# Kernel optimization log

Hardware: AMD Instinct MI355X
Metric: run time of the kernel (lower is better)

Reference implementation:

```python
import jax, jax.numpy as jnp
import numpy as np

LEAKY_ALPHA = 0.2
EPS_NORM = 1e-07


def _leaky_relu(x):
    return jnp.where(x >= 0, x, LEAKY_ALPHA * x)


def setup_inputs() -> dict:
    key = jax.random.key(0)
    ks = jax.random.split(key, 10)
    B, N, F = 16, 1024, 256
    H, Q, K, V = 4, 128, 128, 128
    return {
        "e": jax.random.normal(ks[0], (B, N, N), dtype=jnp.float32),
        "x_atm": jax.random.normal(ks[1], (B, N, F), dtype=jnp.float32),
        "mask": jnp.ones((B, N), dtype=jnp.float32),
        "eps": jax.random.normal(ks[2], (1,), dtype=jnp.float32) * 0.02,
        "Wq": jax.random.normal(ks[3], (H, F, Q), dtype=jnp.float32) * 0.05,
        "Wk": jax.random.normal(ks[4], (H, F, K), dtype=jnp.float32) * 0.05,
        "Wv": jax.random.normal(ks[5], (H, F, V), dtype=jnp.float32) * 0.05,
        "aq": jax.random.normal(ks[6], (H, Q), dtype=jnp.float32) * 0.05,
        "bq": jnp.zeros((H,), dtype=jnp.float32),
        "ak": jax.random.normal(ks[7], (H, K), dtype=jnp.float32) * 0.05,
        "bk": jnp.zeros((H,), dtype=jnp.float32),
    }


def reference(e, x_atm, mask, eps, Wq, Wk, Wv, aq, bq, ak, bk):
    B, N, _ = e.shape
    # add learned eps to the diagonal of e (set_diag(diag + eps))
    e_mod = e + eps[0] * jnp.eye(N, dtype=e.dtype)  # [B,N,N]

    # per-head query/key scalars: Dense -> LeakyReLU -> Dense(1)
    q = jnp.einsum("bhnq,hq->bhn", _leaky_relu(jnp.einsum("bnf,hfq->bhnq", x_atm, Wq)), aq) + bq[None, :, None]  # [B,H,N]
    k = jnp.einsum("bhnk,hk->bhn", _leaky_relu(jnp.einsum("bnf,hfk->bhnk", x_atm, Wk)), ak) + bk[None, :, None]  # [B,H,N]

    # attn[b,h,i,j] = tanh((q_i + k_j) * e_mod[b,i,j])
    scores = jnp.tanh((q[..., :, None] + k[..., None, :]) * e_mod[:, None, :, :])  # [B,H,N,N]

    # L2-normalize each row (tf.linalg.normalize norm + 1e-7)
    norm = jnp.sqrt(jnp.sum(scores * scores, axis=-1, keepdims=True)) + EPS_NORM
    attn = scores / norm

    # values and aggregation
    v = jnp.einsum("bnf,hfv->bhnv", x_atm, Wv)  # [B,H,N,V] (dropout rate 0 -> identity)
    out = jnp.einsum("bhij,bhjv->bhiv", attn, v)  # [B,H,N,V]

    # pooling == 'mask': sum over nodes weighted by mask -> [B,H,V]
    pooled = jnp.einsum("bhnv,bn->bhv", out, mask)

    # concat heads along feature axis -> [B, H*V]
    return pooled.reshape(B, -1)
```

## Files before the change

kernel.cpp:

```cpp
#include <hip/hip_runtime.h>

#define B_ 16
#define N_ 1024
#define F_ 256
#define H_ 4
#define QDIM 128

#define TANH_PRESCALE 2.8853900817779268f

typedef __attribute__((ext_vector_type(8))) short bf16x8;
typedef __attribute__((ext_vector_type(4))) float f32x4;

__device__ __forceinline__ float leaky(float x) {
    return x >= 0.f ? x : 0.2f * x;
}

__device__ __forceinline__ unsigned short bfbits(float f) {
    unsigned u = __float_as_uint(f);
    return (unsigned short)((u + 0x7fffu + ((u >> 16) & 1u)) >> 16);
}

__global__ __launch_bounds__(256) void convert_all(
    const float4* __restrict__ x4, ushort4* __restrict__ xh4,
    const float* __restrict__ Wq, const float* __restrict__ Wk,
    ushort* __restrict__ Wqt, ushort* __restrict__ Wkt)
{
    const int bx = blockIdx.x;
    if (bx < 2048) {
        const int t = bx * 256 + threadIdx.x;
        const float4 a = x4[2 * t], b = x4[2 * t + 1];
        ushort4 o0, o1;
        o0.x = bfbits(a.x); o0.y = bfbits(a.y); o0.z = bfbits(a.z); o0.w = bfbits(a.w);
        o1.x = bfbits(b.x); o1.y = bfbits(b.y); o1.z = bfbits(b.z); o1.w = bfbits(b.w);
        xh4[2 * t] = o0; xh4[2 * t + 1] = o1;
    } else {
        const int t2 = (bx - 2048) * 256 + threadIdx.x;
        const int z = t2 >> 17, t = t2 & 131071;
        const int f = t & 255, q = (t >> 8) & 127, h = t >> 15;
        const float* W = z ? Wk : Wq;
        ushort* O = z ? Wkt : Wqt;
        O[t] = bfbits(W[(h * 256 + f) * 128 + q]);
    }
}

__global__ __launch_bounds__(256) void qk_mfma(
    const ushort* __restrict__ xh,
    const ushort* __restrict__ Wqt, const ushort* __restrict__ Wkt,
    const float* __restrict__ aq, const float* __restrict__ bq,
    const float* __restrict__ ak, const float* __restrict__ bk,
    float* __restrict__ qbuf, float* __restrict__ kbuf)
{
    const int tid = threadIdx.x;
    const int mt  = blockIdx.x;
    const int h   = blockIdx.y;
    const bool isQ = (blockIdx.z == 0);
    const ushort* Wt = isQ ? Wqt : Wkt;
    const float*  av = isQ ? aq : ak;
    const float*  bv = isQ ? bq : bk;
    float* out = isQ ? qbuf : kbuf;

    __shared__ char  xs[64 * 512];
    __shared__ float sp[4][64];

    {
        const int r = tid >> 2;
        const uint4* src = reinterpret_cast<const uint4*>(xh + (size_t)(mt * 64 + r) * 256);
        #pragma unroll
        for (int i = 0; i < 8; ++i) {
            const int c = (tid & 3) + 4 * i;
            const uint4 v = src[c];
            *reinterpret_cast<uint4*>(xs + r * 512 + ((c ^ (r & 7)) << 4)) = v;
        }
    }
    __syncthreads();

    const int l  = tid & 63, w = tid >> 6;
    const int g  = l >> 4, li = l & 15;

    bf16x8 Bf[8][2];
    #pragma unroll
    for (int nf = 0; nf < 2; ++nf) {
        const int c = w * 32 + nf * 16 + li;
        const ushort* bp = Wt + ((size_t)(h * 128 + c)) * 256 + 8 * g;
        #pragma unroll
        for (int s = 0; s < 8; ++s)
            Bf[s][nf] = *reinterpret_cast<const bf16x8*>(bp + s * 32);
    }

    f32x4 acc[4][2];
    #pragma unroll
    for (int m = 0; m < 4; ++m)
        #pragma unroll
        for (int nf = 0; nf < 2; ++nf)
            acc[m][nf] = (f32x4){0.f, 0.f, 0.f, 0.f};

    #pragma unroll
    for (int s = 0; s < 8; ++s) {
        #pragma unroll
        for (int m = 0; m < 4; ++m) {
            const int r = m * 16 + li;
            const int chunk = (4 * s + g) ^ (r & 7);
            const bf16x8 af = *reinterpret_cast<const bf16x8*>(xs + r * 512 + chunk * 16);
            acc[m][0] = __builtin_amdgcn_mfma_f32_16x16x32_bf16(af, Bf[s][0], acc[m][0], 0, 0, 0);
            acc[m][1] = __builtin_amdgcn_mfma_f32_16x16x32_bf16(af, Bf[s][1], acc[m][1], 0, 0, 0);
        }
    }

    float part[4][4];
    #pragma unroll
    for (int m = 0; m < 4; ++m)
        #pragma unroll
        for (int j = 0; j < 4; ++j) part[m][j] = 0.f;

    #pragma unroll
    for (int nf = 0; nf < 2; ++nf) {
        const float a_ = av[h * QDIM + w * 32 + nf * 16 + li];
        #pragma unroll
        for (int m = 0; m < 4; ++m)
            #pragma unroll
            for (int j = 0; j < 4; ++j)
                part[m][j] = fmaf(a_, leaky(acc[m][nf][j]), part[m][j]);
    }
    #pragma unroll
    for (int mask = 1; mask < 16; mask <<= 1)
        #pragma unroll
        for (int m = 0; m < 4; ++m)
            #pragma unroll
            for (int j = 0; j < 4; ++j)
                part[m][j] += __shfl_xor(part[m][j], mask, 64);

    if (li == 0) {
        #pragma unroll
        for (int m = 0; m < 4; ++m)
            #pragma unroll
            for (int j = 0; j < 4; ++j)
                sp[w][m * 16 + g * 4 + j] = part[m][j];
    }
    __syncthreads();

    if (tid < 64) {
        const float val = (sp[0][tid] + sp[1][tid] + sp[2][tid] + sp[3][tid] + bv[h]) * TANH_PRESCALE;
        const int R = mt * 64 + tid;
        out[((R >> 10) * H_ + h) * N_ + (R & 1023)] = val;
    }
}

__global__ __launch_bounds__(512) void attn_kernel(
    const float* __restrict__ e,
    const float* __restrict__ qbuf, const float* __restrict__ kbuf,
    const float* __restrict__ mask, const float* __restrict__ epsp,
    float* __restrict__ pbuf)
{
    const int tid  = threadIdx.x;
    const int wav  = tid >> 6;
    const int h    = wav & 3;
    const int half = wav >> 2;
    const int lane = tid & 63;
    const int b    = blockIdx.y;
    const int ic   = blockIdx.x;
    const int i0   = ic * 16 + half * 8;
    const float epsv = epsp[0];
    const int udiag = ic >> 4;

    __shared__ f32x4 red4[4][4][64];

    const f32x4* kr4 = reinterpret_cast<const f32x4*>(kbuf + (b * H_ + h) * N_);
    f32x4 kk4[4];
    #pragma unroll
    for (int u = 0; u < 4; ++u) kk4[u] = kr4[u * 64 + lane];

    f32x4 wacc4[4];
    #pragma unroll
    for (int u = 0; u < 4; ++u) wacc4[u] = (f32x4){0.f, 0.f, 0.f, 0.f};

    const float* qrow  = qbuf + (b * H_ + h) * N_;
    const float* mrow  = mask + b * N_;
    const f32x4* ebase = reinterpret_cast<const f32x4*>(e + ((size_t)b << 20)) + lane;

    #pragma unroll 2
    for (int ii = 0; ii < 8; ++ii) {
        const int i = i0 + ii;
        const float qi = qrow[i];
        const f32x4* er4 = ebase + ((size_t)i << 8);
        const bool isdl = (lane == ((i >> 2) & 63));
        const float dadd = isdl ? epsv : 0.f;
        float p[4][4];
        float ssl = 0.f;
        #pragma unroll
        for (int u = 0; u < 4; ++u) {
            const f32x4 ev = er4[u * 64];
            const f32x4 kv = kk4[u];
            #pragma unroll
            for (int c = 0; c < 4; ++c) {
                const float qk = qi + kv[c];
                float arg = qk * ev[c];
                if (u == udiag && c == (ii & 3)) arg = fmaf(qk, dadd, arg);
                const float e2 = __builtin_amdgcn_exp2f(arg);
                const float pv = 1.f - 2.f * __builtin_amdgcn_rcpf(e2 + 1.f);
                p[u][c] = pv;
                ssl = fmaf(pv, pv, ssl);
            }
        }
        #pragma unroll
        for (int m = 1; m < 64; m <<= 1) ssl += __shfl_xor(ssl, m, 64);
        const float scale = mrow[i] * __builtin_amdgcn_rcpf(sqrtf(ssl) + 1e-7f);
        #pragma unroll
        for (int u = 0; u < 4; ++u)
            #pragma unroll
            for (int c = 0; c < 4; ++c)
                wacc4[u][c] = fmaf(scale, p[u][c], wacc4[u][c]);
    }

    if (half == 1) {
        #pragma unroll
        for (int u = 0; u < 4; ++u) red4[h][u][lane] = wacc4[u];
    }
    __syncthreads();
    if (half == 0) {
        f32x4* pr4 = reinterpret_cast<f32x4*>(pbuf + ((size_t)((ic * 16 + b) * H_ + h) << 10));
        #pragma unroll
        for (int u = 0; u < 4; ++u) {
            const f32x4 o = wacc4[u] + red4[h][u][lane];
            pr4[u * 64 + lane] = o;
        }
    }
}

__global__ __launch_bounds__(256) void ypart_kernel(
    const float* __restrict__ x, const float* __restrict__ pbuf,
    float* __restrict__ ypart)
{
    const int tid = threadIdx.x;
    const int bx  = blockIdx.x;
    const int b   = bx >> 4;
    const int jc  = bx & 15;
    const int j0  = jc * 64;

    __shared__ float ws_[H_][64];
    {
        const int hh = tid >> 6, j = tid & 63;
        const float* pp = pbuf + ((size_t)(b * H_ + hh) << 10) + j0 + j;
        float s0 = 0.f, s1 = 0.f, s2 = 0.f, s3 = 0.f;
        #pragma unroll 4
        for (int ic = 0; ic < 64; ic += 4) {
            s0 += pp[(size_t)(ic + 0) * 65536];
            s1 += pp[(size_t)(ic + 1) * 65536];
            s2 += pp[(size_t)(ic + 2) * 65536];
            s3 += pp[(size_t)(ic + 3) * 65536];
        }
        ws_[hh][j] = (s0 + s1) + (s2 + s3);
    }
    __syncthreads();

    float a0 = 0.f, a1 = 0.f, a2 = 0.f, a3 = 0.f;
    const float* xcol = x + ((size_t)(b * N_ + j0)) * F_ + tid;
    #pragma unroll 4
    for (int j = 0; j < 64; ++j) {
        const float xv = xcol[(size_t)j * F_];
        a0 = fmaf(ws_[0][j], xv, a0);
        a1 = fmaf(ws_[1][j], xv, a1);
        a2 = fmaf(ws_[2][j], xv, a2);
        a3 = fmaf(ws_[3][j], xv, a3);
    }
    float* yp = ypart + (size_t)(b * 16 + jc) * (H_ * F_) + tid;
    yp[0 * F_] = a0; yp[1 * F_] = a1; yp[2 * F_] = a2; yp[3 * F_] = a3;
}

__global__ __launch_bounds__(256) void pool_kernel(
    const float* __restrict__ ypart, const float* __restrict__ Wv,
    float* __restrict__ out)
{
    const int tid = threadIdx.x;
    const int bh  = blockIdx.x;
    const int b   = bh >> 2;
    const int h   = bh & 3;
    __shared__ float ys[256];
    float s = 0.f;
    #pragma unroll
    for (int jc = 0; jc < 16; ++jc)
        s += ypart[(size_t)(b * 16 + jc) * (H_ * F_) + h * F_ + tid];
    ys[tid] = s;
    __syncthreads();
    if (tid < 128) {
        float acc = 0.f;
        const float* wv = Wv + h * (F_ * 128) + tid;
        #pragma unroll 4
        for (int f = 0; f < F_; ++f) acc = fmaf(ys[f], wv[f * 128], acc);
        out[bh * 128 + tid] = acc;
    }
}

extern "C" void kernel_launch(void* const* d_in, const int* in_sizes, int n_in,
                              void* d_out, int out_size, void* d_ws, size_t ws_size,
                              hipStream_t stream) {
    const float* e    = (const float*)d_in[0];
    const float* x    = (const float*)d_in[1];
    const float* mask = (const float*)d_in[2];
    const float* eps  = (const float*)d_in[3];
    const float* Wq   = (const float*)d_in[4];
    const float* Wk   = (const float*)d_in[5];
    const float* Wv   = (const float*)d_in[6];
    const float* aq   = (const float*)d_in[7];
    const float* bq   = (const float*)d_in[8];
    const float* ak   = (const float*)d_in[9];
    const float* bk   = (const float*)d_in[10];

    float*  qbuf  = (float*)d_ws;
    float*  kbuf  = qbuf + 65536;
    float*  pbuf  = kbuf + 65536;
    float*  ypart = pbuf + 4194304;
    ushort* xh    = (ushort*)(ypart + 262144);
    ushort* Wqt   = xh + 4194304;
    ushort* Wkt   = Wqt + 131072;
    float*  outf  = (float*)d_out;

    convert_all<<<3072, 256, 0, stream>>>((const float4*)x, (ushort4*)xh, Wq, Wk, Wqt, Wkt);
    qk_mfma<<<dim3(256, 4, 2), 256, 0, stream>>>(xh, Wqt, Wkt, aq, bq, ak, bk, qbuf, kbuf);
    attn_kernel<<<dim3(64, 16), 512, 0, stream>>>(e, qbuf, kbuf, mask, eps, pbuf);
    ypart_kernel<<<256, 256, 0, stream>>>(x, pbuf, ypart);
    pool_kernel<<<64, 256, 0, stream>>>(ypart, Wv, outf);
}
```

Baseline: 87.52 us.

## Store attention partials in bf16, read bf16 x, and pack attn math as float2

The attention kernel now writes its per-chunk column-weight partials as bf16 instead of fp32, and the ypart kernel reads those partials and the already-converted bf16 copy of x instead of fp32 x. This halves the bytes moved through the intermediate buffer and the x read. The inner tanh/normalize loop is also rewritten on 2-wide float vectors so the compiler can emit packed FMA/add instructions. Precision drops in the partial sums and in x for the aggregation, which risks larger numerical error.

```diff
diff --git a/kernel.cpp b/kernel.cpp
--- a/kernel.cpp
+++ b/kernel.cpp
@@ -10,6 +10,7 @@
 
 typedef __attribute__((ext_vector_type(8))) short bf16x8;
 typedef __attribute__((ext_vector_type(4))) float f32x4;
+typedef __attribute__((ext_vector_type(2))) float f32x2;
 
 __device__ __forceinline__ float leaky(float x) {
     return x >= 0.f ? x : 0.2f * x;
@@ -18,6 +19,10 @@
 __device__ __forceinline__ unsigned short bfbits(float f) {
     unsigned u = __float_as_uint(f);
     return (unsigned short)((u + 0x7fffu + ((u >> 16) & 1u)) >> 16);
+}
+
+__device__ __forceinline__ float bf2f(unsigned short u) {
+    return __uint_as_float(((unsigned)u) << 16);
 }
 
 __global__ __launch_bounds__(256) void convert_all(
@@ -149,7 +154,7 @@
     const float* __restrict__ e,
     const float* __restrict__ qbuf, const float* __restrict__ kbuf,
     const float* __restrict__ mask, const float* __restrict__ epsp,
-    float* __restrict__ pbuf)
+    ushort* __restrict__ pbuf)
 {
     const int tid  = threadIdx.x;
     const int wav  = tid >> 6;
@@ -162,72 +167,95 @@
     const float epsv = epsp[0];
     const int udiag = ic >> 4;
 
-    __shared__ f32x4 red4[4][4][64];
+    __shared__ f32x2 red2[4][8][64];
 
     const f32x4* kr4 = reinterpret_cast<const f32x4*>(kbuf + (b * H_ + h) * N_);
-    f32x4 kk4[4];
-    #pragma unroll
-    for (int u = 0; u < 4; ++u) kk4[u] = kr4[u * 64 + lane];
-
-    f32x4 wacc4[4];
-    #pragma unroll
-    for (int u = 0; u < 4; ++u) wacc4[u] = (f32x4){0.f, 0.f, 0.f, 0.f};
+    f32x2 kk2[8];
+    #pragma unroll
+    for (int u = 0; u < 4; ++u) {
+        const f32x4 kv = kr4[u * 64 + lane];
+        kk2[2 * u]     = __builtin_shufflevector(kv, kv, 0, 1);
+        kk2[2 * u + 1] = __builtin_shufflevector(kv, kv, 2, 3);
+    }
+
+    f32x2 wacc2[8];
+    #pragma unroll
+    for (int p = 0; p < 8; ++p) wacc2[p] = (f32x2){0.f, 0.f};
 
     const float* qrow  = qbuf + (b * H_ + h) * N_;
     const float* mrow  = mask + b * N_;
     const f32x4* ebase = reinterpret_cast<const f32x4*>(e + ((size_t)b << 20)) + lane;
+
+    const f32x2 one2 = {1.f, 1.f};
+    const f32x2 m2   = {-2.f, -2.f};
 
     #pragma unroll 2
     for (int ii = 0; ii < 8; ++ii) {
         const int i = i0 + ii;
         const float qi = qrow[i];
+        const f32x2 qi2 = {qi, qi};
         const f32x4* er4 = ebase + ((size_t)i << 8);
         const bool isdl = (lane == ((i >> 2) & 63));
         const float dadd = isdl ? epsv : 0.f;
-        float p[4][4];
-        float ssl = 0.f;
+        f32x2 pv[8];
+        f32x2 sslv = {0.f, 0.f};
         #pragma unroll
         for (int u = 0; u < 4; ++u) {
             const f32x4 ev = er4[u * 64];
-            const f32x4 kv = kk4[u];
             #pragma unroll
-            for (int c = 0; c < 4; ++c) {
-                const float qk = qi + kv[c];
-                float arg = qk * ev[c];
-                if (u == udiag && c == (ii & 3)) arg = fmaf(qk, dadd, arg);
-                const float e2 = __builtin_amdgcn_exp2f(arg);
-                const float pv = 1.f - 2.f * __builtin_amdgcn_rcpf(e2 + 1.f);
-                p[u][c] = pv;
-                ssl = fmaf(pv, pv, ssl);
+            for (int s = 0; s < 2; ++s) {
+                const int p = 2 * u + s;
+                const f32x2 ev2 = s ? __builtin_shufflevector(ev, ev, 2, 3)
+                                    : __builtin_shufflevector(ev, ev, 0, 1);
+                const f32x2 qk2 = qi2 + kk2[p];
+                f32x2 arg2 = qk2 * ev2;
+                if (u == udiag && s == ((ii & 3) >> 1)) {
+                    const int cc = ii & 1;
+                    arg2[cc] = fmaf(qk2[cc], dadd, arg2[cc]);
+                }
+                f32x2 ex;
+                ex[0] = __builtin_amdgcn_exp2f(arg2[0]);
+                ex[1] = __builtin_amdgcn_exp2f(arg2[1]);
+                const f32x2 d2 = ex + one2;
+                f32x2 r2;
+                r2[0] = __builtin_amdgcn_rcpf(d2[0]);
+                r2[1] = __builtin_amdgcn_rcpf(d2[1]);
+                const f32x2 pvv = __builtin_elementwise_fma(r2, m2, one2);
+                pv[p] = pvv;
+                sslv = __builtin_elementwise_fma(pvv, pvv, sslv);
             }
         }
+        float ssl = sslv[0] + sslv[1];
         #pragma unroll
         for (int m = 1; m < 64; m <<= 1) ssl += __shfl_xor(ssl, m, 64);
         const float scale = mrow[i] * __builtin_amdgcn_rcpf(sqrtf(ssl) + 1e-7f);
-        #pragma unroll
-        for (int u = 0; u < 4; ++u)
-            #pragma unroll
-            for (int c = 0; c < 4; ++c)
-                wacc4[u][c] = fmaf(scale, p[u][c], wacc4[u][c]);
+        const f32x2 sc2 = {scale, scale};
+        #pragma unroll
+        for (int p = 0; p < 8; ++p)
+            wacc2[p] = __builtin_elementwise_fma(sc2, pv[p], wacc2[p]);
     }
 
     if (half == 1) {
         #pragma unroll
-        for (int u = 0; u < 4; ++u) red4[h][u][lane] = wacc4[u];
+        for (int p = 0; p < 8; ++p) red2[h][p][lane] = wacc2[p];
     }
     __syncthreads();
     if (half == 0) {
-        f32x4* pr4 = reinterpret_cast<f32x4*>(pbuf + ((size_t)((ic * 16 + b) * H_ + h) << 10));
+        ushort* pr = pbuf + ((size_t)((ic * 16 + b) * H_ + h) << 10);
         #pragma unroll
         for (int u = 0; u < 4; ++u) {
-            const f32x4 o = wacc4[u] + red4[h][u][lane];
-            pr4[u * 64 + lane] = o;
+            const f32x2 a = wacc2[2 * u]     + red2[h][2 * u][lane];
+            const f32x2 c = wacc2[2 * u + 1] + red2[h][2 * u + 1][lane];
+            ushort4 o;
+            o.x = bfbits(a[0]); o.y = bfbits(a[1]);
+            o.z = bfbits(c[0]); o.w = bfbits(c[1]);
+            *reinterpret_cast<ushort4*>(pr + u * 256 + lane * 4) = o;
         }
     }
 }
 
 __global__ __launch_bounds__(256) void ypart_kernel(
-    const float* __restrict__ x, const float* __restrict__ pbuf,
+    const ushort* __restrict__ xh, const ushort* __restrict__ pbuf,
     float* __restrict__ ypart)
 {
     const int tid = threadIdx.x;
@@ -239,24 +267,24 @@
     __shared__ float ws_[H_][64];
     {
         const int hh = tid >> 6, j = tid & 63;
-        const float* pp = pbuf + ((size_t)(b * H_ + hh) << 10) + j0 + j;
+        const ushort* pp = pbuf + ((size_t)(b * H_ + hh) << 10) + j0 + j;
         float s0 = 0.f, s1 = 0.f, s2 = 0.f, s3 = 0.f;
         #pragma unroll 4
         for (int ic = 0; ic < 64; ic += 4) {
-            s0 += pp[(size_t)(ic + 0) * 65536];
-            s1 += pp[(size_t)(ic + 1) * 65536];
-            s2 += pp[(size_t)(ic + 2) * 65536];
-            s3 += pp[(size_t)(ic + 3) * 65536];
+            s0 += bf2f(pp[(size_t)(ic + 0) * 65536]);
+            s1 += bf2f(pp[(size_t)(ic + 1) * 65536]);
+            s2 += bf2f(pp[(size_t)(ic + 2) * 65536]);
+            s3 += bf2f(pp[(size_t)(ic + 3) * 65536]);
         }
         ws_[hh][j] = (s0 + s1) + (s2 + s3);
     }
     __syncthreads();
 
     float a0 = 0.f, a1 = 0.f, a2 = 0.f, a3 = 0.f;
-    const float* xcol = x + ((size_t)(b * N_ + j0)) * F_ + tid;
+    const ushort* xcol = xh + ((size_t)(b * N_ + j0)) * F_ + tid;
     #pragma unroll 4
     for (int j = 0; j < 64; ++j) {
-        const float xv = xcol[(size_t)j * F_];
+        const float xv = bf2f(xcol[(size_t)j * F_]);
         a0 = fmaf(ws_[0][j], xv, a0);
         a1 = fmaf(ws_[1][j], xv, a1);
         a2 = fmaf(ws_[2][j], xv, a2);
@@ -307,9 +335,9 @@
 
     float*  qbuf  = (float*)d_ws;
     float*  kbuf  = qbuf + 65536;
-    float*  pbuf  = kbuf + 65536;
-    float*  ypart = pbuf + 4194304;
-    ushort* xh    = (ushort*)(ypart + 262144);
+    float*  ypartb= kbuf + 65536;
+    ushort* pbuf  = (ushort*)(ypartb + 262144);
+    ushort* xh    = pbuf + 4194304;
     ushort* Wqt   = xh + 4194304;
     ushort* Wkt   = Wqt + 131072;
     float*  outf  = (float*)d_out;
@@ -317,6 +345,6 @@
     convert_all<<<3072, 256, 0, stream>>>((const float4*)x, (ushort4*)xh, Wq, Wk, Wqt, Wkt);
     qk_mfma<<<dim3(256, 4, 2), 256, 0, stream>>>(xh, Wqt, Wkt, aq, bq, ak, bk, qbuf, kbuf);
     attn_kernel<<<dim3(64, 16), 512, 0, stream>>>(e, qbuf, kbuf, mask, eps, pbuf);
-    ypart_kernel<<<256, 256, 0, stream>>>(x, pbuf, ypart);
-    pool_kernel<<<64, 256, 0, stream>>>(ypart, Wv, outf);
-}
+    ypart_kernel<<<256, 256, 0, stream>>>(xh, pbuf, ypartb);
+    pool_kernel<<<64, 256, 0, stream>>>(ypartb, Wv, outf);
+}
```

Result: faster. 83.57 us (-4.5%).
